# Optimization experiments

Measured on AMD Instinct MI355X. Metric: run time of the kernel, lower is better.

## Reference

```python
import jax, jax.numpy as jnp
import numpy as np

B, S, IN = 8, 512, 128
D, H, DK, DV, DFF, L = 512, 8, 64, 64, 2048, 4
LOCAL = 64
EPS = 1e-5


def setup_inputs() -> dict:
    key = jax.random.key(0)
    ks = jax.random.split(key, 12)
    w = lambda k, shape: (jax.random.normal(k, shape, jnp.float32) * 0.02)
    return dict(
        x=jax.random.normal(ks[0], (B, S, IN), jnp.float32),
        We=w(ks[1], (IN, D)), be=jnp.zeros((D,), jnp.float32),
        Wq=w(ks[2], (L, D, H * DK)), bq=jnp.zeros((L, H * DK), jnp.float32),
        Wk=w(ks[3], (L, D, H * DK)), bk=jnp.zeros((L, H * DK), jnp.float32),
        Wv=w(ks[4], (L, D, H * DV)), bv=jnp.zeros((L, H * DV), jnp.float32),
        Wo=w(ks[5], (L, H * DV, D)), bo=jnp.zeros((L, D), jnp.float32),
        ln1_g=jnp.ones((L, D), jnp.float32), ln1_b=jnp.zeros((L, D), jnp.float32),
        W1=w(ks[6], (L, D, DFF)), b1=jnp.zeros((L, DFF), jnp.float32),
        W2=w(ks[7], (L, DFF, D)), b2=jnp.zeros((L, D), jnp.float32),
        ln2_g=jnp.ones((L, D), jnp.float32), ln2_b=jnp.zeros((L, D), jnp.float32),
    )


def _layernorm(x, g, b):
    m = jnp.mean(x, -1, keepdims=True)
    v = jnp.mean((x - m) ** 2, -1, keepdims=True)
    return (x - m) / jnp.sqrt(v + EPS) * g + b


def _gelu(x):
    # GELU tanh approximation exactly as in the torch module
    return 0.5 * x * (1.0 + jnp.tanh(np.sqrt(2.0 / np.pi) * (x + 0.044715 * x ** 3)))


def _sincos_pe():
    pos = jnp.arange(S, dtype=jnp.float32)[:, None]
    div = jnp.exp(jnp.arange(0, D, 2, dtype=jnp.float32) * (-np.log(10000.0) / D))
    pe = jnp.zeros((S, D), jnp.float32)
    pe = pe.at[:, 0::2].set(jnp.sin(pos * div))
    pe = pe.at[:, 1::2].set(jnp.cos(pos * div))
    return pe


def _forward(x, We, be, Wq, bq, Wk, bk, Wv, bv, Wo, bo,
             ln1_g, ln1_b, W1, b1, W2, b2, ln2_g, ln2_b):
    h = x @ We + be + _sincos_pe()  # [B,S,D]
    idx = jnp.arange(S)
    # local band mask: positions farther than LOCAL are masked with -1e9
    mask = jnp.abs(idx[:, None] - idx[None, :]) > LOCAL  # [S,S] bool

    def mha(hin, l):
        q = (hin @ Wq[l] + bq[l]).reshape(B, S, H, DK).transpose(0, 2, 1, 3)
        k = (hin @ Wk[l] + bk[l]).reshape(B, S, H, DK).transpose(0, 2, 1, 3)
        v = (hin @ Wv[l] + bv[l]).reshape(B, S, H, DV).transpose(0, 2, 1, 3)
        scores = jnp.einsum('bhqd,bhkd->bhqk', q, k) / np.sqrt(DK)
        scores = jnp.where(mask, -1e9, scores)
        a = jax.nn.softmax(scores, axis=-1)
        ctx = jnp.einsum('bhqk,bhkd->bhqd', a, v)
        ctx = ctx.transpose(0, 2, 1, 3).reshape(B, S, H * DV)
        out = ctx @ Wo[l] + bo[l]
        return _layernorm(out + hin, ln1_g[l], ln1_b[l]), a

    attns = []
    for l in range(L):
        h, a = mha(h, l)
        h, a = mha(h, l)  # local=True: second pass with the SAME weights
        ff = _gelu(h @ W1[l] + b1[l]) @ W2[l] + b2[l]
        h = _layernorm(ff + h, ln2_g[l], ln2_b[l])
        attns.append(a)
    attns = jnp.stack(attns).transpose(1, 0, 2, 3, 4)  # [B,L,H,S,S]
    return h, attns


def reference(x, We, be, Wq, bq, Wk, bk, Wv, bv, Wo, bo,
              ln1_g, ln1_b, W1, b1, W2, b2, ln2_g, ln2_b):
    return _forward(x, We, be, Wq, bq, Wk, bk, Wv, bv, Wo, bo,
                    ln1_g, ln1_b, W1, b1, W2, b2, ln2_g, ln2_b)
```

## Files before the change

### kernel.cpp

```cpp
#include <hip/hip_runtime.h>

using bf16 = __bf16;
using bf16x8 = __attribute__((ext_vector_type(8))) __bf16;
using bf16x4 = __attribute__((ext_vector_type(4))) __bf16;
using f32x4  = __attribute__((ext_vector_type(4))) float;

#define AS1(p) ((const __attribute__((address_space(1))) unsigned int*)(p))
#define AS3(p) ((__attribute__((address_space(3))) unsigned int*)(p))

template<int N> __device__ __forceinline__ void wait_vmcnt() {
    if constexpr (N == 0) asm volatile("s_waitcnt vmcnt(0)" ::: "memory");
    else if constexpr (N == 3) asm volatile("s_waitcnt vmcnt(3)" ::: "memory");
    else if constexpr (N == 4) asm volatile("s_waitcnt vmcnt(4)" ::: "memory");
    else if constexpr (N == 6) asm volatile("s_waitcnt vmcnt(6)" ::: "memory");
    else if constexpr (N == 8) asm volatile("s_waitcnt vmcnt(8)" ::: "memory");
}

template<int TM, int TN, int EPI>
__global__ __launch_bounds__(256, TM == 64 ? 4 : 3)
void gemm_kernel(const bf16* __restrict__ A, const bf16* __restrict__ WT,
                 const float* __restrict__ bias, bf16* __restrict__ Cbf,
                 const float* __restrict__ PE,
                 int K, int ldc, int gx, int q8)
{
    constexpr int NA  = TM / 16;
    constexpr int NCH = NA + TN / 16;
    constexpr int CPW = NCH / 4;
    constexpr int MI  = TM / 32;
    constexpr int NI  = TN / 32;
    constexpr int ASZ = TM * 32;
    constexpr int BSZ = TN * 32;
    __shared__ bf16 Asm[3 * ASZ];
    __shared__ bf16 Bsm[3 * BSZ];
    const int tid = threadIdx.x;
    const int lane = tid & 63;
    const int w  = tid >> 6;
    const int wr = w >> 1, wc = w & 1;
    const int l4 = lane & 15, lg = lane >> 4;

    const int bid = blockIdx.x;
    const int s  = (bid & 7) * q8 + (bid >> 3);
    const int by = s / gx, bx = s - by * gx;
    const size_t m0 = (size_t)by * TM;
    const size_t n0 = (size_t)bx * TN;

    f32x4 acc[MI][NI] = {};

    const int lr  = lane >> 2;
    const int ksw = (((lane & 3) ^ ((lane >> 3) & 3)) * 8);
    const bf16* src[CPW];
    bf16* dst0[CPW];
    int step[CPW];
    #pragma unroll
    for (int ci = 0; ci < CPW; ++ci) {
        const int c = w * CPW + ci;
        if (c < NA) {
            src[ci]  = A + (m0 + (size_t)(c * 16 + lr)) * K + ksw;
            dst0[ci] = Asm + c * 512;
            step[ci] = ASZ;
        } else {
            src[ci]  = WT + (n0 + (size_t)((c - NA) * 16 + lr)) * K + ksw;
            dst0[ci] = Bsm + (c - NA) * 512;
            step[ci] = BSZ;
        }
    }
    const int rsw = (lg ^ ((l4 >> 1) & 3)) * 8;
    const bf16* Ar = &Asm[(wr * (TM / 2) + l4) * 32 + rsw];
    const bf16* Br = &Bsm[(wc * (TN / 2) + l4) * 32 + rsw];

    auto STAGE = [&](int b) {
        #pragma unroll
        for (int ci = 0; ci < CPW; ++ci) {
            __builtin_amdgcn_global_load_lds(AS1(src[ci]),
                                             AS3(dst0[ci] + b * step[ci]), 16, 0, 0);
            src[ci] += 32;
        }
    };

    const int nt = K >> 5;
    STAGE(0);
    if (nt > 1) STAGE(1);

    int cur = 0;
    for (int t = 0; t < nt; ++t) {
        if (t + 2 < nt) {
            int pb = cur - 1; if (pb < 0) pb = 2;
            STAGE(pb);
            wait_vmcnt<2 * CPW>();
        } else if (t + 1 < nt) {
            wait_vmcnt<CPW>();
        } else {
            wait_vmcnt<0>();
        }
        __builtin_amdgcn_s_barrier();
        const bf16* Ac = Ar + cur * ASZ;
        const bf16* Bc = Br + cur * BSZ;
        bf16x8 aF[MI], bF[NI];
        #pragma unroll
        for (int i = 0; i < MI; ++i) aF[i] = *(const bf16x8*)(Ac + i * 512);
        #pragma unroll
        for (int i = 0; i < NI; ++i) bF[i] = *(const bf16x8*)(Bc + i * 512);
        #pragma unroll
        for (int mi = 0; mi < MI; ++mi)
            #pragma unroll
            for (int ni = 0; ni < NI; ++ni)
                acc[mi][ni] = __builtin_amdgcn_mfma_f32_16x16x32_bf16(
                    aF[mi], bF[ni], acc[mi][ni], 0, 0, 0);
        asm volatile("s_waitcnt lgkmcnt(0)" ::: "memory");
        __builtin_amdgcn_s_barrier();
        cur = (cur == 2) ? 0 : cur + 1;
    }

    #pragma unroll
    for (int ni = 0; ni < NI; ++ni) {
        const int col = (int)n0 + wc * (TN / 2) + ni * 16 + l4;
        const float bv = bias[col];
        #pragma unroll
        for (int mi = 0; mi < MI; ++mi) {
            const int row0 = (int)m0 + wr * (TM / 2) + mi * 16 + lg * 4;
            #pragma unroll
            for (int r = 0; r < 4; ++r) {
                float v = acc[mi][ni][r] + bv;
                const int row = row0 + r;
                if (EPI == 1) {
                    float u = 1.5957691216057308f * (v + 0.044715f * v * v * v);
                    v = v / (1.0f + __expf(-u));
                }
                if (EPI == 2) {
                    v += PE[((row & 511) << 9) + col];
                }
                Cbf[(size_t)row * ldc + col] = (bf16)v;
            }
        }
    }
}

template<int WRITE_ATTN>
__global__ __launch_bounds__(256, 3)
void attn_kernel(const bf16* __restrict__ qkv, bf16* __restrict__ ctx,
                 float* __restrict__ attn_out )
{
    __shared__ bf16 KPs[192 * 72];
    __shared__ bf16 Vt[64 * 200];
    bf16* Ks = KPs;
    bf16* Ps = KPs;
    const int tid = threadIdx.x;
    const int lane = tid & 63, w = tid >> 6;
    const int l4 = lane & 15, lg = lane >> 4;
    const int bh = blockIdx.y, ib = blockIdx.x;
    const int b = bh >> 3, hd = bh & 7;
    const int i0 = ib * 64;
    const int j0 = (i0 >= 64) ? i0 - 64 : 0;
    const int j1 = (i0 + 128 <= 512) ? i0 + 128 : 512;
    const int W = j1 - j0;
    const size_t rowb = (size_t)b * 512;

    if (WRITE_ATTN) {
        float* arow = attn_out + (size_t)b * 8388608 + (size_t)hd * 262144 +
                      (size_t)i0 * 512;
        const int zr = tid >> 2, p = tid & 3;
        f32x4 z = {0.f, 0.f, 0.f, 0.f};
        f32x4* rp = (f32x4*)(arow + (size_t)zr * 512);
        for (int c = p; c < (j0 >> 2); c += 4) rp[c] = z;
        for (int c = (j1 >> 2) + p; c < 128; c += 4) rp[c] = z;
    }

    for (int it = 0; it < 6; ++it) {
        int chunk = tid + it * 256;
        int j = chunk >> 3, k0 = (chunk & 7) * 8;
        if (j < W) {
            bf16x8 v = *(const bf16x8*)(qkv + (rowb + j0 + j) * 1536 + 512 + hd * 64 + k0);
            *(bf16x8*)(&Ks[j * 72 + k0]) = v;
        }
    }
    for (int it = 0; it < 6; ++it) {
        int chunk = tid + it * 256;
        int j = chunk >> 3, d0 = (chunk & 7) * 8;
        if (j < W) {
            bf16x8 v = *(const bf16x8*)(qkv + (rowb + j0 + j) * 1536 + 1024 + hd * 64 + d0);
            #pragma unroll
            for (int e = 0; e < 8; ++e) Vt[(d0 + e) * 200 + j] = v[e];
        }
    }
    bf16x8 qF0, qF1;
    {
        const bf16* qrow = qkv + (rowb + i0 + w * 16 + l4) * 1536 + hd * 64;
        qF0 = *(const bf16x8*)(qrow + lg * 8);
        qF1 = *(const bf16x8*)(qrow + 32 + lg * 8);
    }
    __syncthreads();

    f32x4 s[12];
    #pragma unroll
    for (int t = 0; t < 12; ++t) s[t] = (f32x4){0.f, 0.f, 0.f, 0.f};
    const int NT = W >> 4;
    __builtin_amdgcn_s_setprio(1);
    for (int t = 0; t < NT; ++t) {
        const bf16* kb = &Ks[(t * 16 + l4) * 72];
        bf16x8 b0 = *(const bf16x8*)(kb + lg * 8);
        bf16x8 b1 = *(const bf16x8*)(kb + 32 + lg * 8);
        s[t] = __builtin_amdgcn_mfma_f32_16x16x32_bf16(qF0, b0, s[t], 0, 0, 0);
        s[t] = __builtin_amdgcn_mfma_f32_16x16x32_bf16(qF1, b1, s[t], 0, 0, 0);
    }
    __builtin_amdgcn_s_setprio(0);
    const int irow0 = i0 + w * 16 + lg * 4;
    float pm[4] = {-3e38f, -3e38f, -3e38f, -3e38f};
    for (int t = 0; t < NT; ++t) {
        int jg = j0 + t * 16 + l4;
        #pragma unroll
        for (int r = 0; r < 4; ++r) {
            int dd = irow0 + r - jg;
            float sv = s[t][r] * 0.125f;
            if (dd > 64 || dd < -64) sv = -1e30f;
            s[t][r] = sv;
            pm[r] = fmaxf(pm[r], sv);
        }
    }
    #pragma unroll
    for (int d = 1; d < 16; d <<= 1)
        #pragma unroll
        for (int r = 0; r < 4; ++r) pm[r] = fmaxf(pm[r], __shfl_xor(pm[r], d));
    float ps[4] = {0.f, 0.f, 0.f, 0.f};
    for (int t = 0; t < NT; ++t)
        #pragma unroll
        for (int r = 0; r < 4; ++r) {
            float p = __expf(s[t][r] - pm[r]);
            s[t][r] = p;
            ps[r] += p;
        }
    #pragma unroll
    for (int d = 1; d < 16; d <<= 1)
        #pragma unroll
        for (int r = 0; r < 4; ++r) ps[r] += __shfl_xor(ps[r], d);
    float rinv[4];
    #pragma unroll
    for (int r = 0; r < 4; ++r) rinv[r] = 1.0f / ps[r];

    __syncthreads();

    for (int t = 0; t < NT; ++t) {
        #pragma unroll
        for (int r = 0; r < 4; ++r) {
            float p = s[t][r] * rinv[r];
            Ps[(w * 16 + lg * 4 + r) * 200 + t * 16 + l4] = (bf16)p;
            if (WRITE_ATTN) {
                size_t off = (size_t)b * 8388608 + (size_t)hd * 262144 +
                             (size_t)(i0 + w * 16 + lg * 4 + r) * 512 +
                             (size_t)(j0 + t * 16 + l4);
                attn_out[off] = p;
            }
        }
    }
    f32x4 o[4] = {};
    const int KS = W >> 5;
    __builtin_amdgcn_s_setprio(1);
    for (int ks = 0; ks < KS; ++ks) {
        bf16x8 aF = *(const bf16x8*)(&Ps[(w * 16 + l4) * 200 + ks * 32 + lg * 8]);
        #pragma unroll
        for (int ni = 0; ni < 4; ++ni) {
            bf16x8 bF = *(const bf16x8*)(&Vt[(ni * 16 + l4) * 200 + ks * 32 + lg * 8]);
            o[ni] = __builtin_amdgcn_mfma_f32_16x16x32_bf16(aF, bF, o[ni], 0, 0, 0);
        }
    }
    __builtin_amdgcn_s_setprio(0);
    __syncthreads();
    bf16* Cs = Vt;
    #pragma unroll
    for (int ni = 0; ni < 4; ++ni)
        #pragma unroll
        for (int r = 0; r < 4; ++r)
            Cs[(w * 16 + lg * 4 + r) * 64 + ni * 16 + l4] = (bf16)o[ni][r];
    __syncthreads();
    #pragma unroll
    for (int it = 0; it < 2; ++it) {
        int chunk = tid + it * 256;
        int rl = chunk >> 3, c0 = (chunk & 7) << 3;
        *(bf16x8*)(&ctx[(rowb + i0 + rl) * 512 + hd * 64 + c0]) =
            *(const bf16x8*)(&Cs[rl * 64 + c0]);
    }
}

__global__ __launch_bounds__(256)
void ln_kernel(const bf16* __restrict__ y, const bf16* __restrict__ hin,
               const float* __restrict__ g, const float* __restrict__ bb,
               bf16* __restrict__ hbf, float* __restrict__ hf)
{
    const int row = blockIdx.x * 4 + (threadIdx.x >> 6);
    const int lane = threadIdx.x & 63;
    const size_t base = (size_t)row * 512 + lane * 8;
    bf16x8 yv = *(const bf16x8*)(y + base);
    bf16x8 hv = *(const bf16x8*)(hin + base);
    float x[8];
    #pragma unroll
    for (int i = 0; i < 8; ++i) x[i] = (float)yv[i] + (float)hv[i];
    float s = 0.f, q = 0.f;
    #pragma unroll
    for (int i = 0; i < 8; ++i) { s += x[i]; q += x[i] * x[i]; }
    #pragma unroll
    for (int d = 1; d < 64; d <<= 1) { s += __shfl_xor(s, d); q += __shfl_xor(q, d); }
    const float m = s * 0.001953125f;
    const float var = q * 0.001953125f - m * m;
    const float rstd = rsqrtf(var + 1e-5f);
    const int c0 = lane * 8;
    f32x4 g0 = *(const f32x4*)(g + c0), g1v = *(const f32x4*)(g + c0 + 4);
    f32x4 b0 = *(const f32x4*)(bb + c0), b1v = *(const f32x4*)(bb + c0 + 4);
    float o[8];
    #pragma unroll
    for (int i = 0; i < 8; ++i) {
        float gg = i < 4 ? g0[i] : g1v[i - 4];
        float bv = i < 4 ? b0[i] : b1v[i - 4];
        o[i] = (x[i] - m) * rstd * gg + bv;
    }
    if (hf) {
        f32x4 o0, o1;
        #pragma unroll
        for (int i = 0; i < 4; ++i) { o0[i] = o[i]; o1[i] = o[i + 4]; }
        *(f32x4*)(hf + base) = o0;
        *(f32x4*)(hf + base + 4) = o1;
    } else {
        bf16x8 ob;
        #pragma unroll
        for (int i = 0; i < 8; ++i) ob[i] = (bf16)o[i];
        *(bf16x8*)(hbf + base) = ob;
    }
}

struct TMat { const float* src; size_t dst; int K; int N; int tile0; };
struct TDesc { TMat m[26]; };

__global__ __launch_bounds__(256)
void wtrans_kernel(TDesc d, bf16* __restrict__ wbuf)
{
    __shared__ float tile[32][33];
    int t = blockIdx.x;
    int mi = 0;
    while (t >= d.m[mi + 1].tile0) ++mi;
    const TMat mm = d.m[mi];
    const int lt = t - mm.tile0;
    const int tpr = mm.N >> 5;
    const int kt = lt / tpr, nt = lt % tpr;
    const int r = threadIdx.x >> 5, c = threadIdx.x & 31;
    #pragma unroll
    for (int it = 0; it < 4; ++it)
        tile[r + it * 8][c] =
            mm.src[(size_t)(kt * 32 + r + it * 8) * mm.N + nt * 32 + c];
    __syncthreads();
    #pragma unroll
    for (int it = 0; it < 4; ++it)
        wbuf[mm.dst + (size_t)(nt * 32 + r + it * 8) * mm.K + kt * 32 + c] =
            (bf16)tile[c][r + it * 8];
}

__global__ void prep_kernel(const float* __restrict__ x, bf16* __restrict__ xbf,
                            float* __restrict__ pe,
                            const float* bq, const float* bk, const float* bv,
                            float* __restrict__ bqkv)
{
    const int bid = blockIdx.x;
    if (bid < 512) {
        int i = bid * 256 + threadIdx.x;
        f32x4 v = *(const f32x4*)(x + (size_t)i * 4);
        bf16x4 o;
        #pragma unroll
        for (int e = 0; e < 4; ++e) o[e] = (bf16)v[e];
        *(bf16x4*)(xbf + (size_t)i * 4) = o;
    } else if (bid < 1024) {
        int i = (bid - 512) * 256 + threadIdx.x;
        int s = i >> 8, d2 = i & 255;
        float ang = (float)s * expf((float)(2 * d2) * -0.017988946039016f);
        pe[(s << 9) + 2 * d2]     = sinf(ang);
        pe[(s << 9) + 2 * d2 + 1] = cosf(ang);
    } else {
        int i = (bid - 1024) * 256 + threadIdx.x;
        if (i < 6144) {
            int l = i / 1536, c = i - l * 1536;
            float v;
            if (c < 512) v = bq[l * 512 + c];
            else if (c < 1024) v = bk[l * 512 + c - 512];
            else v = bv[l * 512 + c - 1024];
            bqkv[i] = v;
        }
    }
}

extern "C" void kernel_launch(void* const* d_in, const int* in_sizes, int n_in,
                              void* d_out, int out_size, void* d_ws, size_t ws_size,
                              hipStream_t stream)
{
    const float* x   = (const float*)d_in[0];
    const float* We  = (const float*)d_in[1];
    const float* be  = (const float*)d_in[2];
    const float* Wq  = (const float*)d_in[3];
    const float* bq  = (const float*)d_in[4];
    const float* Wk  = (const float*)d_in[5];
    const float* bk  = (const float*)d_in[6];
    const float* Wv  = (const float*)d_in[7];
    const float* bv  = (const float*)d_in[8];
    const float* Wo  = (const float*)d_in[9];
    const float* bo  = (const float*)d_in[10];
    const float* g1  = (const float*)d_in[11];
    const float* b1n = (const float*)d_in[12];
    const float* W1  = (const float*)d_in[13];
    const float* b1f = (const float*)d_in[14];
    const float* W2  = (const float*)d_in[15];
    const float* b2f = (const float*)d_in[16];
    const float* g2  = (const float*)d_in[17];
    const float* b2n = (const float*)d_in[18];

    char* ws = (char*)d_ws;
    bf16* wbuf = (bf16*)ws;
    size_t off = 12648448ull * 2;
    float* bqkv = (float*)(ws + off); off += 6144ull * 4;
    float* pe   = (float*)(ws + off); off += 262144ull * 4;
    bf16* xbf   = (bf16*)(ws + off);  off += 524288ull * 2;
    bf16* hbf   = (bf16*)(ws + off);  off += 2097152ull * 2;
    bf16* qkvb  = (bf16*)(ws + off);  off += 6291456ull * 2;
    bf16* ctx   = (bf16*)(ws + off);  off += 2097152ull * 2;
    bf16* tmp   = (bf16*)(ws + off);  off += 2097152ull * 2;
    bf16* ffn   = (bf16*)(ws + off);  off += 8388608ull * 2;
    (void)ws_size; (void)in_sizes; (void)n_in; (void)out_size;

    float* out_h = (float*)d_out;
    float* out_attn = out_h + 2097152;

    TDesc td{};
    int tile = 0, e = 0;
    auto add = [&](const float* src, size_t dst, int K, int N) {
        td.m[e].src = src; td.m[e].dst = dst; td.m[e].K = K; td.m[e].N = N;
        td.m[e].tile0 = tile; tile += (K >> 5) * (N >> 5); ++e;
    };
    add(We, 0, 128, 512);
    for (int l = 0; l < 4; ++l) {
        size_t base = 65536 + (size_t)l * 3145728;
        add(Wq + (size_t)l * 262144,  base + 0,       512, 512);
        add(Wk + (size_t)l * 262144,  base + 262144,  512, 512);
        add(Wv + (size_t)l * 262144,  base + 524288,  512, 512);
        add(Wo + (size_t)l * 262144,  base + 786432,  512, 512);
        add(W1 + (size_t)l * 1048576, base + 1048576, 512, 2048);
        add(W2 + (size_t)l * 1048576, base + 2097152, 2048, 512);
    }
    td.m[e].tile0 = tile;

    wtrans_kernel<<<dim3(tile), dim3(256), 0, stream>>>(td, wbuf);
    prep_kernel<<<dim3(1048), dim3(256), 0, stream>>>(x, xbf, pe, bq, bk, bv, bqkv);

    gemm_kernel<64, 128, 2><<<dim3(256), dim3(256), 0, stream>>>(
        xbf, wbuf, be, hbf, pe, 128, 512, 4, 32);

    for (int l = 0; l < 4; ++l) {
        const bf16* WqkvT = wbuf + 65536 + (size_t)l * 3145728;
        const bf16* WoT   = WqkvT + 786432;
        const bf16* W1T   = WqkvT + 1048576;
        const bf16* W2T   = WqkvT + 2097152;
        for (int pass = 0; pass < 2; ++pass) {
            gemm_kernel<128, 128, 0><<<dim3(384), dim3(256), 0, stream>>>(
                hbf, WqkvT, bqkv + l * 1536, qkvb, (float*)nullptr,
                512, 1536, 12, 48);
            if (pass == 0)
                attn_kernel<0><<<dim3(8, 64), dim3(256), 0, stream>>>(
                    qkvb, ctx, (float*)nullptr);
            else
                attn_kernel<1><<<dim3(8, 64), dim3(256), 0, stream>>>(
                    qkvb, ctx, out_attn + (size_t)l * 2097152);
            gemm_kernel<64, 128, 0><<<dim3(256), dim3(256), 0, stream>>>(
                ctx, WoT, bo + l * 512, tmp, (float*)nullptr,
                512, 512, 4, 32);
            ln_kernel<<<dim3(1024), dim3(256), 0, stream>>>(
                tmp, hbf, g1 + l * 512, b1n + l * 512, hbf, (float*)nullptr);
        }
        gemm_kernel<128, 128, 1><<<dim3(512), dim3(256), 0, stream>>>(
            hbf, W1T, b1f + l * 2048, ffn, (float*)nullptr,
            512, 2048, 16, 64);
        gemm_kernel<64, 128, 0><<<dim3(256), dim3(256), 0, stream>>>(
            ffn, W2T, b2f + l * 512, tmp, (float*)nullptr,
            2048, 512, 4, 32);
        ln_kernel<<<dim3(1024), dim3(256), 0, stream>>>(
            tmp, hbf, g2 + l * 512, b2n + l * 512, hbf,
            (l == 3) ? out_h : (float*)nullptr);
    }
}
```

Baseline: 673.4 us.

## Split-K the Wo and W2 GEMMs and reduce partials in layernorm

The N=512 output GEMMs (Wo projection and FFN down-projection) now run as a two-way split-K grid, with each half writing fp32 partial sums to a workspace buffer. The following layernorm kernel adds the two partials and the bias before the residual add. This doubles the block count on GEMMs that previously launched only 256 blocks, aiming for better CU occupancy. In exchange it adds extra fp32 write and read traffic for the partials.

Measured after the change: 699.1 us. 1.04x slower.

```diff
diff --git a/kernel.cpp b/kernel.cpp
--- a/kernel.cpp
+++ b/kernel.cpp
@@ -20,8 +20,8 @@
 __global__ __launch_bounds__(256, TM == 64 ? 4 : 3)
 void gemm_kernel(const bf16* __restrict__ A, const bf16* __restrict__ WT,
                  const float* __restrict__ bias, bf16* __restrict__ Cbf,
-                 const float* __restrict__ PE,
-                 int K, int ldc, int gx, int q8)
+                 float* __restrict__ Cpart, const float* __restrict__ PE,
+                 int K, int ldc, int gx, int q8, int partOff)
 {
     constexpr int NA  = TM / 16;
     constexpr int NCH = NA + TN / 16;
@@ -44,6 +44,10 @@
     const size_t m0 = (size_t)by * TM;
     const size_t n0 = (size_t)bx * TN;
 
+    const int ks   = (EPI == 3) ? blockIdx.y : 0;
+    const int Keff = (EPI == 3) ? (K >> 1) : K;
+    const int kbase = ks * Keff;
+
     f32x4 acc[MI][NI] = {};
 
     const int lr  = lane >> 2;
@@ -55,11 +59,11 @@
     for (int ci = 0; ci < CPW; ++ci) {
         const int c = w * CPW + ci;
         if (c < NA) {
-            src[ci]  = A + (m0 + (size_t)(c * 16 + lr)) * K + ksw;
+            src[ci]  = A + (m0 + (size_t)(c * 16 + lr)) * K + kbase + ksw;
             dst0[ci] = Asm + c * 512;
             step[ci] = ASZ;
         } else {
-            src[ci]  = WT + (n0 + (size_t)((c - NA) * 16 + lr)) * K + ksw;
+            src[ci]  = WT + (n0 + (size_t)((c - NA) * 16 + lr)) * K + kbase + ksw;
             dst0[ci] = Bsm + (c - NA) * 512;
             step[ci] = BSZ;
         }
@@ -77,7 +81,7 @@
         }
     };
 
-    const int nt = K >> 5;
+    const int nt = Keff >> 5;
     STAGE(0);
     if (nt > 1) STAGE(1);
 
@@ -111,10 +115,11 @@
         cur = (cur == 2) ? 0 : cur + 1;
     }
 
+    float* P = (EPI == 3) ? (Cpart + (size_t)ks * partOff) : nullptr;
     #pragma unroll
     for (int ni = 0; ni < NI; ++ni) {
         const int col = (int)n0 + wc * (TN / 2) + ni * 16 + l4;
-        const float bv = bias[col];
+        const float bv = (EPI == 3) ? 0.f : bias[col];
         #pragma unroll
         for (int mi = 0; mi < MI; ++mi) {
             const int row0 = (int)m0 + wr * (TM / 2) + mi * 16 + lg * 4;
@@ -129,7 +134,11 @@
                 if (EPI == 2) {
                     v += PE[((row & 511) << 9) + col];
                 }
-                Cbf[(size_t)row * ldc + col] = (bf16)v;
+                if (EPI == 3) {
+                    P[(size_t)row * ldc + col] = v;
+                } else {
+                    Cbf[(size_t)row * ldc + col] = (bf16)v;
+                }
             }
         }
     }
@@ -280,19 +289,38 @@
     }
 }
 
+template<int SK>
 __global__ __launch_bounds__(256)
-void ln_kernel(const bf16* __restrict__ y, const bf16* __restrict__ hin,
+void ln_kernel(const bf16* __restrict__ y, const float* __restrict__ part,
+               int partOff, const float* __restrict__ bias,
+               const bf16* __restrict__ hin,
                const float* __restrict__ g, const float* __restrict__ bb,
                bf16* __restrict__ hbf, float* __restrict__ hf)
 {
     const int row = blockIdx.x * 4 + (threadIdx.x >> 6);
     const int lane = threadIdx.x & 63;
     const size_t base = (size_t)row * 512 + lane * 8;
-    bf16x8 yv = *(const bf16x8*)(y + base);
+    const int c0 = lane * 8;
     bf16x8 hv = *(const bf16x8*)(hin + base);
     float x[8];
-    #pragma unroll
-    for (int i = 0; i < 8; ++i) x[i] = (float)yv[i] + (float)hv[i];
+    if (SK) {
+        f32x4 p00 = *(const f32x4*)(part + base);
+        f32x4 p01 = *(const f32x4*)(part + base + 4);
+        f32x4 p10 = *(const f32x4*)(part + partOff + base);
+        f32x4 p11 = *(const f32x4*)(part + partOff + base + 4);
+        f32x4 bi0 = *(const f32x4*)(bias + c0);
+        f32x4 bi1 = *(const f32x4*)(bias + c0 + 4);
+        #pragma unroll
+        for (int i = 0; i < 8; ++i) {
+            float yv = (i < 4) ? (p00[i] + p10[i] + bi0[i])
+                               : (p01[i - 4] + p11[i - 4] + bi1[i - 4]);
+            x[i] = yv + (float)hv[i];
+        }
+    } else {
+        bf16x8 yv = *(const bf16x8*)(y + base);
+        #pragma unroll
+        for (int i = 0; i < 8; ++i) x[i] = (float)yv[i] + (float)hv[i];
+    }
     float s = 0.f, q = 0.f;
     #pragma unroll
     for (int i = 0; i < 8; ++i) { s += x[i]; q += x[i] * x[i]; }
@@ -301,7 +329,6 @@
     const float m = s * 0.001953125f;
     const float var = q * 0.001953125f - m * m;
     const float rstd = rsqrtf(var + 1e-5f);
-    const int c0 = lane * 8;
     f32x4 g0 = *(const f32x4*)(g + c0), g1v = *(const f32x4*)(g + c0 + 4);
     f32x4 b0 = *(const f32x4*)(bb + c0), b1v = *(const f32x4*)(bb + c0 + 4);
     float o[8];
@@ -416,7 +443,7 @@
     bf16* hbf   = (bf16*)(ws + off);  off += 2097152ull * 2;
     bf16* qkvb  = (bf16*)(ws + off);  off += 6291456ull * 2;
     bf16* ctx   = (bf16*)(ws + off);  off += 2097152ull * 2;
-    bf16* tmp   = (bf16*)(ws + off);  off += 2097152ull * 2;
+    float* part = (float*)(ws + off); off += 4194304ull * 4;
     bf16* ffn   = (bf16*)(ws + off);  off += 8388608ull * 2;
     (void)ws_size; (void)in_sizes; (void)n_in; (void)out_size;
 
@@ -445,7 +472,7 @@
     prep_kernel<<<dim3(1048), dim3(256), 0, stream>>>(x, xbf, pe, bq, bk, bv, bqkv);
 
     gemm_kernel<64, 128, 2><<<dim3(256), dim3(256), 0, stream>>>(
-        xbf, wbuf, be, hbf, pe, 128, 512, 4, 32);
+        xbf, wbuf, be, hbf, (float*)nullptr, pe, 128, 512, 4, 32, 0);
 
     for (int l = 0; l < 4; ++l) {
         const bf16* WqkvT = wbuf + 65536 + (size_t)l * 3145728;
@@ -454,28 +481,30 @@
         const bf16* W2T   = WqkvT + 2097152;
         for (int pass = 0; pass < 2; ++pass) {
             gemm_kernel<128, 128, 0><<<dim3(384), dim3(256), 0, stream>>>(
-                hbf, WqkvT, bqkv + l * 1536, qkvb, (float*)nullptr,
-                512, 1536, 12, 48);
+                hbf, WqkvT, bqkv + l * 1536, qkvb, (float*)nullptr, (float*)nullptr,
+                512, 1536, 12, 48, 0);
             if (pass == 0)
                 attn_kernel<0><<<dim3(8, 64), dim3(256), 0, stream>>>(
                     qkvb, ctx, (float*)nullptr);
             else
                 attn_kernel<1><<<dim3(8, 64), dim3(256), 0, stream>>>(
                     qkvb, ctx, out_attn + (size_t)l * 2097152);
-            gemm_kernel<64, 128, 0><<<dim3(256), dim3(256), 0, stream>>>(
-                ctx, WoT, bo + l * 512, tmp, (float*)nullptr,
-                512, 512, 4, 32);
-            ln_kernel<<<dim3(1024), dim3(256), 0, stream>>>(
-                tmp, hbf, g1 + l * 512, b1n + l * 512, hbf, (float*)nullptr);
+            gemm_kernel<64, 128, 3><<<dim3(256, 2), dim3(256), 0, stream>>>(
+                ctx, WoT, (float*)nullptr, (bf16*)nullptr, part, (float*)nullptr,
+                512, 512, 4, 32, 2097152);
+            ln_kernel<1><<<dim3(1024), dim3(256), 0, stream>>>(
+                (bf16*)nullptr, part, 2097152, bo + l * 512, hbf,
+                g1 + l * 512, b1n + l * 512, hbf, (float*)nullptr);
         }
         gemm_kernel<128, 128, 1><<<dim3(512), dim3(256), 0, stream>>>(
-            hbf, W1T, b1f + l * 2048, ffn, (float*)nullptr,
-            512, 2048, 16, 64);
-        gemm_kernel<64, 128, 0><<<dim3(256), dim3(256), 0, stream>>>(
-            ffn, W2T, b2f + l * 512, tmp, (float*)nullptr,
-            2048, 512, 4, 32);
-        ln_kernel<<<dim3(1024), dim3(256), 0, stream>>>(
-            tmp, hbf, g2 + l * 512, b2n + l * 512, hbf,
+            hbf, W1T, b1f + l * 2048, ffn, (float*)nullptr, (float*)nullptr,
+            512, 2048, 16, 64, 0);
+        gemm_kernel<64, 128, 3><<<dim3(256, 2), dim3(256), 0, stream>>>(
+            ffn, W2T, (float*)nullptr, (bf16*)nullptr, part, (float*)nullptr,
+            2048, 512, 4, 32, 2097152);
+        ln_kernel<1><<<dim3(1024), dim3(256), 0, stream>>>(
+            (bf16*)nullptr, part, 2097152, b2f + l * 512, hbf,
+            g2 + l * 512, b2n + l * 512, hbf,
             (l == 3) ? out_h : (float*)nullptr);
     }
 }
```
